# Kernel tuning notes

Measured on AMD Instinct MI355X. Metric: run time of the kernel, lower is better.

## Reference

```python
import jax, jax.numpy as jnp
import numpy as np

L, H = 3, 2048  # stacked LSTM cells, uniform width


def setup_inputs() -> dict:
    key = jax.random.key(0)
    ks = jax.random.split(key, 7)
    s = 1.0 / np.sqrt(H)  # torch default LSTM init scale
    x = jax.random.normal(ks[0], (H,), jnp.float32)
    W_ih = jax.random.normal(ks[1], (L, 4 * H, H), jnp.float32) * s
    W_hh = jax.random.normal(ks[2], (L, 4 * H, H), jnp.float32) * s
    b_ih = jax.random.normal(ks[3], (L, 4 * H), jnp.float32) * s
    b_hh = jax.random.normal(ks[4], (L, 4 * H), jnp.float32) * s
    h0 = jax.random.uniform(ks[5], (L, H), jnp.float32)  # th.rand init
    c0 = jax.random.uniform(ks[6], (L, H), jnp.float32)
    return {"x": x, "W_ih": W_ih, "W_hh": W_hh, "b_ih": b_ih, "b_hh": b_hh, "h0": h0, "c0": c0}


def reference(x, W_ih, W_hh, b_ih, b_hh, h0, c0):
    # Single-step (seq_len=1, batch=1) LSTM cell applied through L stacked layers;
    # output h of layer l is the input x of layer l+1. Gate order: i, f, g, o.
    def step(xcar, layer):
        Wi, Wh, bi, bh, h, c = layer
        gates = Wi @ xcar + Wh @ h + bi + bh          # [4H]
        i_, f_, g_, o_ = jnp.split(gates, 4)
        i_ = jax.nn.sigmoid(i_)
        f_ = jax.nn.sigmoid(f_)
        g_ = jnp.tanh(g_)
        o_ = jax.nn.sigmoid(o_)
        c_new = f_ * c + i_ * g_
        h_new = o_ * jnp.tanh(c_new)
        return h_new, None

    out, _ = jax.lax.scan(step, x, (W_ih, W_hh, b_ih, b_hh, h0, c0))
    return out.reshape(1, 1, -1)  # torch LSTM returns [seq=1, batch=1, H]
```

## Files before the change

kernel.cpp:

```cpp
#include <hip/hip_runtime.h>
#include <math.h>

#define H 2048
#define G4 (4 * H)

__global__ __launch_bounds__(256) void lstm_gates_kernel(
    const float* __restrict__ Wi,
    const float* __restrict__ Wh,
    const float* __restrict__ bi,
    const float* __restrict__ bh,
    const float* __restrict__ x,
    const float* __restrict__ h,
    float* __restrict__ gates)
{
    const int wave = (blockIdx.x * blockDim.x + threadIdx.x) >> 6;
    const int lane = threadIdx.x & 63;
    if (wave >= G4) return;

    const float4* wi4 = (const float4*)(Wi + (size_t)wave * H);
    const float4* wh4 = (const float4*)(Wh + (size_t)wave * H);
    const float4* x4  = (const float4*)x;
    const float4* h4  = (const float4*)h;

    float acc = 0.f;
#pragma unroll
    for (int it = 0; it < (H / 4) / 64; ++it) {
        const int idx = it * 64 + lane;
        float4 a = wi4[idx];
        float4 v = x4[idx];
        acc += a.x * v.x + a.y * v.y + a.z * v.z + a.w * v.w;
        float4 b = wh4[idx];
        float4 u = h4[idx];
        acc += b.x * u.x + b.y * u.y + b.z * u.z + b.w * u.w;
    }

#pragma unroll
    for (int off = 32; off > 0; off >>= 1)
        acc += __shfl_down(acc, off);

    if (lane == 0)
        gates[wave] = acc + bi[wave] + bh[wave];
}

__global__ __launch_bounds__(256) void lstm_update_kernel(
    const float* __restrict__ gates,
    const float* __restrict__ c0,
    float* __restrict__ h_next,
    float* __restrict__ out_extra)
{
    const int j = blockIdx.x * blockDim.x + threadIdx.x;
    if (j >= H) return;

    const float gi = gates[j];
    const float gf = gates[H + j];
    const float gg = gates[2 * H + j];
    const float go = gates[3 * H + j];

    const float i_ = 1.f / (1.f + expf(-gi));
    const float f_ = 1.f / (1.f + expf(-gf));
    const float g_ = tanhf(gg);
    const float o_ = 1.f / (1.f + expf(-go));

    const float c_new = f_ * c0[j] + i_ * g_;
    const float h_new = o_ * tanhf(c_new);

    h_next[j] = h_new;
    if (out_extra) out_extra[j] = h_new;
}

extern "C" void kernel_launch(void* const* d_in, const int* in_sizes, int n_in,
                              void* d_out, int out_size, void* d_ws, size_t ws_size,
                              hipStream_t stream) {
    const float* x    = (const float*)d_in[0];
    const float* W_ih = (const float*)d_in[1];
    const float* W_hh = (const float*)d_in[2];
    const float* b_ih = (const float*)d_in[3];
    const float* b_hh = (const float*)d_in[4];
    const float* h0   = (const float*)d_in[5];
    const float* c0   = (const float*)d_in[6];
    float* out = (float*)d_out;

    float* gates = (float*)d_ws;
    float* xbuf  = gates + G4;

    const size_t Wstride = (size_t)G4 * H;

    const float* cur_x = x;
    for (int l = 0; l < 3; ++l) {
        const bool last = (l == 2);
        lstm_gates_kernel<<<G4 / 4, 256, 0, stream>>>(
            W_ih + l * Wstride, W_hh + l * Wstride,
            b_ih + (size_t)l * G4, b_hh + (size_t)l * G4,
            cur_x, h0 + (size_t)l * H, gates);

        lstm_update_kernel<<<H / 256, 256, 0, stream>>>(
            gates, c0 + (size_t)l * H,
            last ? out : xbuf,
            nullptr);

        cur_x = xbuf;
    }
}
```

Measured before the change: 412.3 us.

## Hoist all recurrent W_hh matvecs into one upfront launch, one block per row

The W_hh·h products for all three layers, plus layer 0's W_ih·x, do not depend on earlier layers, so they are computed together in a single large launch. Only the dependent W_ih·x products stay on the serial layer chain. Each row is now reduced by a full 256-thread block, with a shared-memory combine, instead of one wave per row. This shortens the serial critical path and gives the first kernel much more parallel memory traffic, at the cost of extra workspace and a block-wide sync per row.

```diff
diff --git a/kernel.cpp b/kernel.cpp
--- a/kernel.cpp
+++ b/kernel.cpp
@@ -2,70 +2,101 @@
 #include <math.h>
 
 #define H 2048
-#define G4 (4 * H)
+#define R (4 * H)
+#define L 3
 
-__global__ __launch_bounds__(256) void lstm_gates_kernel(
-    const float* __restrict__ Wi,
+
+__device__ __forceinline__ float block_row_dot(const float* __restrict__ row,
+                                               const float* __restrict__ vec,
+                                               int t) {
+    const float4* r4 = (const float4*)row;
+    const float4* v4 = (const float4*)vec;
+    float acc = 0.f;
+#pragma unroll
+    for (int it = 0; it < (H / 4) / 256; ++it) {
+        const int idx = it * 256 + t;
+        float4 a = r4[idx];
+        float4 v = v4[idx];
+        acc += a.x * v.x + a.y * v.y + a.z * v.z + a.w * v.w;
+    }
+#pragma unroll
+    for (int off = 32; off > 0; off >>= 1)
+        acc += __shfl_down(acc, off);
+    __shared__ float s[4];
+    if ((t & 63) == 0) s[t >> 6] = acc;
+    __syncthreads();
+    return s[0] + s[1] + s[2] + s[3];
+}
+
+__global__ __launch_bounds__(256) void phase1_kernel(
+    const float* __restrict__ Wi0,
     const float* __restrict__ Wh,
     const float* __restrict__ bi,
     const float* __restrict__ bh,
     const float* __restrict__ x,
-    const float* __restrict__ h,
-    float* __restrict__ gates)
+    const float* __restrict__ h0,
+    float* __restrict__ xpart,
+    float* __restrict__ pre)
 {
-    const int wave = (blockIdx.x * blockDim.x + threadIdx.x) >> 6;
-    const int lane = threadIdx.x & 63;
-    if (wave >= G4) return;
+    const int blk = blockIdx.x;
+    const int t = threadIdx.x;
 
-    const float4* wi4 = (const float4*)(Wi + (size_t)wave * H);
-    const float4* wh4 = (const float4*)(Wh + (size_t)wave * H);
-    const float4* x4  = (const float4*)x;
-    const float4* h4  = (const float4*)h;
-
-    float acc = 0.f;
-#pragma unroll
-    for (int it = 0; it < (H / 4) / 64; ++it) {
-        const int idx = it * 64 + lane;
-        float4 a = wi4[idx];
-        float4 v = x4[idx];
-        acc += a.x * v.x + a.y * v.y + a.z * v.z + a.w * v.w;
-        float4 b = wh4[idx];
-        float4 u = h4[idx];
-        acc += b.x * u.x + b.y * u.y + b.z * u.z + b.w * u.w;
+    const float* row;
+    const float* vec;
+    if (blk < R) {
+        row = Wi0 + (size_t)blk * H;
+        vec = x;
+    } else {
+        const int r = blk - R;
+        const int l = r >> 13;
+        row = Wh + (size_t)r * H;
+        vec = h0 + l * H;
     }
 
-#pragma unroll
-    for (int off = 32; off > 0; off >>= 1)
-        acc += __shfl_down(acc, off);
+    const float tot = block_row_dot(row, vec, t);
 
-    if (lane == 0)
-        gates[wave] = acc + bi[wave] + bh[wave];
+    if (t == 0) {
+        if (blk < R) {
+            xpart[blk] = tot;
+        } else {
+            const int r = blk - R;
+            pre[r] = tot + bi[r] + bh[r];
+        }
+    }
 }
 
-__global__ __launch_bounds__(256) void lstm_update_kernel(
-    const float* __restrict__ gates,
-    const float* __restrict__ c0,
-    float* __restrict__ h_next,
-    float* __restrict__ out_extra)
+__global__ __launch_bounds__(256) void wix_kernel(
+    const float* __restrict__ Wi,
+    const float* __restrict__ x,
+    float* __restrict__ xpart)
+{
+    const int blk = blockIdx.x;
+    const int t = threadIdx.x;
+    const float tot = block_row_dot(Wi + (size_t)blk * H, x, t);
+    if (t == 0) xpart[blk] = tot;
+}
+
+__global__ __launch_bounds__(256) void update_kernel(
+    const float* __restrict__ pre_l,
+    const float* __restrict__ xpart,
+    const float* __restrict__ c0_l,
+    float* __restrict__ h_out)
 {
     const int j = blockIdx.x * blockDim.x + threadIdx.x;
     if (j >= H) return;
 
-    const float gi = gates[j];
-    const float gf = gates[H + j];
-    const float gg = gates[2 * H + j];
-    const float go = gates[3 * H + j];
+    const float gi = pre_l[j]         + xpart[j];
+    const float gf = pre_l[H + j]     + xpart[H + j];
+    const float gg = pre_l[2 * H + j] + xpart[2 * H + j];
+    const float go = pre_l[3 * H + j] + xpart[3 * H + j];
 
     const float i_ = 1.f / (1.f + expf(-gi));
     const float f_ = 1.f / (1.f + expf(-gf));
     const float g_ = tanhf(gg);
     const float o_ = 1.f / (1.f + expf(-go));
 
-    const float c_new = f_ * c0[j] + i_ * g_;
-    const float h_new = o_ * tanhf(c_new);
-
-    h_next[j] = h_new;
-    if (out_extra) out_extra[j] = h_new;
+    const float c_new = f_ * c0_l[j] + i_ * g_;
+    h_out[j] = o_ * tanhf(c_new);
 }
 
 extern "C" void kernel_launch(void* const* d_in, const int* in_sizes, int n_in,
@@ -80,24 +111,21 @@
     const float* c0   = (const float*)d_in[6];
     float* out = (float*)d_out;
 
-    float* gates = (float*)d_ws;
-    float* xbuf  = gates + G4;
+    float* xpart = (float*)d_ws;
+    float* pre   = xpart + R;
+    float* xbuf1 = pre + L * R;
+    float* xbuf2 = xbuf1 + H;
 
-    const size_t Wstride = (size_t)G4 * H;
+    const size_t Wstride = (size_t)R * H;
 
-    const float* cur_x = x;
-    for (int l = 0; l < 3; ++l) {
-        const bool last = (l == 2);
-        lstm_gates_kernel<<<G4 / 4, 256, 0, stream>>>(
-            W_ih + l * Wstride, W_hh + l * Wstride,
-            b_ih + (size_t)l * G4, b_hh + (size_t)l * G4,
-            cur_x, h0 + (size_t)l * H, gates);
+    phase1_kernel<<<R + L * R, 256, 0, stream>>>(
+        W_ih, W_hh, b_ih, b_hh, x, h0, xpart, pre);
 
-        lstm_update_kernel<<<H / 256, 256, 0, stream>>>(
-            gates, c0 + (size_t)l * H,
-            last ? out : xbuf,
-            nullptr);
+    update_kernel<<<H / 256, 256, 0, stream>>>(pre, xpart, c0, xbuf1);
 
-        cur_x = xbuf;
-    }
+    wix_kernel<<<R, 256, 0, stream>>>(W_ih + Wstride, xbuf1, xpart);
+    update_kernel<<<H / 256, 256, 0, stream>>>(pre + R, xpart, c0 + H, xbuf2);
+
+    wix_kernel<<<R, 256, 0, stream>>>(W_ih + 2 * Wstride, xbuf2, xpart);
+    update_kernel<<<H / 256, 256, 0, stream>>>(pre + 2 * R, xpart, c0 + 2 * H, out);
 }
```

New measurement: 396.6 us. 1.04x faster.

## Hoist all W_hh matvecs into one wide launch and fuse cell update into next layer

Applied to the files above, without the earlier changes.

Because the W_hh·h products and biases do not depend on the previous layer, they are computed for all three layers, together with layer 0's W_ih·x, in a single wide launch. Each later layer's W_ih matvec kernel first recomputes the previous layer's cell update into shared memory, then does the dot products. The aim is to cut the serial chain of small launches and fill the GPU with more independent weight streaming. The cost is that every block redundantly recomputes the 2048-element activation vector, and there are extra workspace buffers.

```diff
diff --git a/kernel.cpp b/kernel.cpp
--- a/kernel.cpp
+++ b/kernel.cpp
@@ -1,71 +1,132 @@
 #include <hip/hip_runtime.h>
 #include <math.h>
 
-#define H 2048
-#define G4 (4 * H)
+#define H  2048
+#define R  8192
+#define NT 256
 
-__global__ __launch_bounds__(256) void lstm_gates_kernel(
-    const float* __restrict__ Wi,
+__device__ __forceinline__ void fma4(float4& a, const float4 m, const float4 v) {
+    a.x = fmaf(m.x, v.x, a.x); a.y = fmaf(m.y, v.y, a.y);
+    a.z = fmaf(m.z, v.z, a.z); a.w = fmaf(m.w, v.w, a.w);
+}
+__device__ __forceinline__ float hsum4(const float4 a) {
+    return (a.x + a.y) + (a.z + a.w);
+}
+__device__ __forceinline__ float sigmoidf_(float v) {
+    return 1.f / (1.f + expf(-v));
+}
+
+__global__ __launch_bounds__(NT, 4) void phase1_kernel(
+    const float* __restrict__ Wi0,
     const float* __restrict__ Wh,
     const float* __restrict__ bi,
     const float* __restrict__ bh,
     const float* __restrict__ x,
-    const float* __restrict__ h,
-    float* __restrict__ gates)
+    const float* __restrict__ h0,
+    float* __restrict__ xpA,
+    float* __restrict__ pre)
 {
-    const int wave = (blockIdx.x * blockDim.x + threadIdx.x) >> 6;
+    const int w    = blockIdx.x * (NT / 64) + (threadIdx.x >> 6);
     const int lane = threadIdx.x & 63;
-    if (wave >= G4) return;
+    const int g0   = w * 2;
 
-    const float4* wi4 = (const float4*)(Wi + (size_t)wave * H);
-    const float4* wh4 = (const float4*)(Wh + (size_t)wave * H);
-    const float4* x4  = (const float4*)x;
-    const float4* h4  = (const float4*)h;
-
-    float acc = 0.f;
-#pragma unroll
-    for (int it = 0; it < (H / 4) / 64; ++it) {
-        const int idx = it * 64 + lane;
-        float4 a = wi4[idx];
-        float4 v = x4[idx];
-        acc += a.x * v.x + a.y * v.y + a.z * v.z + a.w * v.w;
-        float4 b = wh4[idx];
-        float4 u = h4[idx];
-        acc += b.x * u.x + b.y * u.y + b.z * u.z + b.w * u.w;
+    const float* row0;
+    const float* vec;
+    if (g0 < R) {
+        row0 = Wi0 + (size_t)g0 * H;
+        vec  = x;
+    } else {
+        const int r = g0 - R;
+        row0 = Wh + (size_t)r * H;
+        vec  = h0 + (r >> 13) * H;
     }
 
+    const float4* r04 = (const float4*)row0;
+    const float4* r14 = (const float4*)(row0 + H);
+    const float4* v4  = (const float4*)vec;
+
+    float4 a0 = {0.f, 0.f, 0.f, 0.f}, a1 = {0.f, 0.f, 0.f, 0.f};
 #pragma unroll
-    for (int off = 32; off > 0; off >>= 1)
-        acc += __shfl_down(acc, off);
+    for (int it = 0; it < 8; ++it) {
+        const int idx = it * 64 + lane;
+        const float4 v  = v4[idx];
+        const float4 m0 = r04[idx];
+        const float4 m1 = r14[idx];
+        fma4(a0, m0, v);
+        fma4(a1, m1, v);
+    }
 
-    if (lane == 0)
-        gates[wave] = acc + bi[wave] + bh[wave];
+    float s0 = hsum4(a0), s1 = hsum4(a1);
+#pragma unroll
+    for (int off = 32; off > 0; off >>= 1) {
+        s0 += __shfl_down(s0, off);
+        s1 += __shfl_down(s1, off);
+    }
+
+    if (lane == 0) {
+        if (g0 < R) {
+            xpA[g0]     = s0;
+            xpA[g0 + 1] = s1;
+        } else {
+            const int r = g0 - R;
+            pre[r]     = s0 + bi[r]     + bh[r];
+            pre[r + 1] = s1 + bi[r + 1] + bh[r + 1];
+        }
+    }
 }
 
-__global__ __launch_bounds__(256) void lstm_update_kernel(
-    const float* __restrict__ gates,
-    const float* __restrict__ c0,
-    float* __restrict__ h_next,
-    float* __restrict__ out_extra)
+__global__ __launch_bounds__(NT, 4) void wix_fused_kernel(
+    const float* __restrict__ Wi_l,
+    const float* __restrict__ pre_lm1,
+    const float* __restrict__ xp_lm1,
+    const float* __restrict__ c_lm1,
+    float* __restrict__ xp_out)
 {
-    const int j = blockIdx.x * blockDim.x + threadIdx.x;
+    __shared__ float hvec[H];
+    const int t = threadIdx.x;
+
+#pragma unroll
+    for (int j = t; j < H; j += NT) {
+        const float gi = pre_lm1[j]         + xp_lm1[j];
+        const float gf = pre_lm1[H + j]     + xp_lm1[H + j];
+        const float gg = pre_lm1[2 * H + j] + xp_lm1[2 * H + j];
+        const float go = pre_lm1[3 * H + j] + xp_lm1[3 * H + j];
+        const float c_new = sigmoidf_(gf) * c_lm1[j] + sigmoidf_(gi) * tanhf(gg);
+        hvec[j] = sigmoidf_(go) * tanhf(c_new);
+    }
+    __syncthreads();
+
+    const int w    = blockIdx.x * (NT / 64) + (t >> 6);
+    const int lane = t & 63;
+    const float4* m4 = (const float4*)(Wi_l + (size_t)w * H);
+    const float4* v4 = (const float4*)hvec;
+
+    float4 a = {0.f, 0.f, 0.f, 0.f};
+#pragma unroll
+    for (int it = 0; it < 8; ++it) {
+        const int idx = it * 64 + lane;
+        fma4(a, m4[idx], v4[idx]);
+    }
+    float s = hsum4(a);
+#pragma unroll
+    for (int off = 32; off > 0; off >>= 1) s += __shfl_down(s, off);
+    if (lane == 0) xp_out[w] = s;
+}
+
+__global__ __launch_bounds__(NT) void final_kernel(
+    const float* __restrict__ pre_2,
+    const float* __restrict__ xpC,
+    const float* __restrict__ c_2,
+    float* __restrict__ out)
+{
+    const int j = blockIdx.x * NT + threadIdx.x;
     if (j >= H) return;
-
-    const float gi = gates[j];
-    const float gf = gates[H + j];
-    const float gg = gates[2 * H + j];
-    const float go = gates[3 * H + j];
-
-    const float i_ = 1.f / (1.f + expf(-gi));
-    const float f_ = 1.f / (1.f + expf(-gf));
-    const float g_ = tanhf(gg);
-    const float o_ = 1.f / (1.f + expf(-go));
-
-    const float c_new = f_ * c0[j] + i_ * g_;
-    const float h_new = o_ * tanhf(c_new);
-
-    h_next[j] = h_new;
-    if (out_extra) out_extra[j] = h_new;
+    const float gi = pre_2[j]         + xpC[j];
+    const float gf = pre_2[H + j]     + xpC[H + j];
+    const float gg = pre_2[2 * H + j] + xpC[2 * H + j];
+    const float go = pre_2[3 * H + j] + xpC[3 * H + j];
+    const float c_new = sigmoidf_(gf) * c_2[j] + sigmoidf_(gi) * tanhf(gg);
+    out[j] = sigmoidf_(go) * tanhf(c_new);
 }
 
 extern "C" void kernel_launch(void* const* d_in, const int* in_sizes, int n_in,
@@ -80,24 +141,20 @@
     const float* c0   = (const float*)d_in[6];
     float* out = (float*)d_out;
 
-    float* gates = (float*)d_ws;
-    float* xbuf  = gates + G4;
+    float* xpA = (float*)d_ws;
+    float* xpB = xpA + R;
+    float* xpC = xpB + R;
+    float* pre = xpC + R;
 
-    const size_t Wstride = (size_t)G4 * H;
+    const size_t Ws = (size_t)R * H;
 
-    const float* cur_x = x;
-    for (int l = 0; l < 3; ++l) {
-        const bool last = (l == 2);
-        lstm_gates_kernel<<<G4 / 4, 256, 0, stream>>>(
-            W_ih + l * Wstride, W_hh + l * Wstride,
-            b_ih + (size_t)l * G4, b_hh + (size_t)l * G4,
-            cur_x, h0 + (size_t)l * H, gates);
+    phase1_kernel<<<4096, NT, 0, stream>>>(W_ih, W_hh, b_ih, b_hh, x, h0,
+                                           xpA, pre);
 
-        lstm_update_kernel<<<H / 256, 256, 0, stream>>>(
-            gates, c0 + (size_t)l * H,
-            last ? out : xbuf,
-            nullptr);
+    wix_fused_kernel<<<2048, NT, 0, stream>>>(W_ih + Ws, pre, xpA, c0, xpB);
 
-        cur_x = xbuf;
-    }
+    wix_fused_kernel<<<2048, NT, 0, stream>>>(W_ih + 2 * Ws, pre + R, xpB,
+                                              c0 + H, xpC);
+
+    final_kernel<<<H / NT, NT, 0, stream>>>(pre + 2 * R, xpC, c0 + 2 * H, out);
 }
```

Measured after the change: 415.9 us. About the same (+0.9%).
